# Kernel tuning notes

Hardware: AMD Instinct MI355X
Metric: run time of the kernel (lower is better)

Reference implementation:

```python
import jax, jax.numpy as jnp
import numpy as np

B, T, D, H, L = 32, 1024, 512, 512, 2
OUT = 512 * 2  # output_size is doubled in setup() (bidirectional)


def setup_inputs() -> dict:
    key = jax.random.key(0)
    ks = jax.random.split(key, 9)
    s = 1.0 / np.sqrt(H)
    return {
        "x": jax.random.normal(ks[0], (B, T, D), jnp.float32),
        "h0": jnp.zeros((L, B, H), jnp.float32),
        "c0": jnp.zeros((L, B, H), jnp.float32),
        # stacked LSTM weights, gate order (i, f, g, o) as in flax LSTMCell
        "Wi_f": jax.random.normal(ks[1], (L, D, 4 * H), jnp.float32) * s,
        "Wh_f": jax.random.normal(ks[2], (L, H, 4 * H), jnp.float32) * s,
        "b_f": jnp.zeros((L, 4 * H), jnp.float32),
        "Wi_b": jax.random.normal(ks[3], (L, D, 4 * H), jnp.float32) * s,
        "Wh_b": jax.random.normal(ks[4], (L, H, 4 * H), jnp.float32) * s,
        "b_b": jnp.zeros((L, 4 * H), jnp.float32),
        "W_out": jax.random.normal(ks[5], (2 * H, OUT), jnp.float32) * s,
        "b_out": jnp.zeros((OUT,), jnp.float32),
    }


def _lstm_layer(xs, h0, c0, Wi, Wh, b):
    # xs: [T, B, Din]; scans the sequential recurrence
    def step(carry, x_t):
        h, c = carry
        gates = x_t @ Wi + h @ Wh + b  # [B, 4H]
        i, f, g, o = jnp.split(gates, 4, axis=-1)
        c = jax.nn.sigmoid(f) * c + jax.nn.sigmoid(i) * jnp.tanh(g)
        h = jax.nn.sigmoid(o) * jnp.tanh(c)
        return (h, c), h

    _, hs = jax.lax.scan(step, (h0, c0), xs)
    return hs  # [T, B, H]


def _stack(xs, h0, c0, Wi, Wh, b):
    h = xs
    for l in range(Wi.shape[0]):  # small fixed layer loop
        h = _lstm_layer(h, h0[l], c0[l], Wi[l], Wh[l], b[l])
    return h


def reference(x, h0, c0, Wi_f, Wh_f, b_f, Wi_b, Wh_b, b_b, W_out, b_out):
    xs = jnp.swapaxes(x, 0, 1)  # [T, B, D]
    hf = _stack(xs, h0, c0, Wi_f, Wh_f, b_f)                # forward in time
    hb = _stack(xs[::-1], h0, c0, Wi_b, Wh_b, b_b)[::-1]    # backward in time
    out = jax.nn.relu(jnp.concatenate([hf, hb], axis=-1)) @ W_out + b_out
    return jnp.swapaxes(out, 0, 1)  # [B, T, 2*output_size]
```

## Files before the change

### kernel.cpp

```cpp
#include <hip/hip_runtime.h>
#include <math.h>

typedef __bf16 bf16;
typedef __bf16 bf16x8 __attribute__((ext_vector_type(8)));
typedef float f32x4 __attribute__((ext_vector_type(4)));
typedef int i32x4 __attribute__((ext_vector_type(4)));
typedef unsigned int u32;

#define TT 1024
#define BB 32
#define DD 512
#define HH 512
#define NG4 2048

#define OFF_FLAGS 0ull
#define FLAG_INTS (4u*1024u*64u)
#define OFF_ABORT ((size_t)FLAG_INTS*4ull)
#define OFF_WBT   (OFF_ABORT + 1024ull)
#define OFF_PL    (OFF_WBT + 2097152ull)
#define PL_BYTES  32768ull
#define OFF_H1    (OFF_PL + 4ull*2ull*16ull*PL_BYTES)
#define FULL_ELEM ((size_t)(TT+1)*BB*HH)

#define PLP(gg, pp, slot) (ws + OFF_PL + (((size_t)((gg)*2+(pp))*16 + (size_t)(slot))*PL_BYTES))

__device__ __forceinline__ bf16x8 load16_sc(const void* p) {
  i32x4 r;
  asm volatile("global_load_dwordx4 %0, %1, off sc0 sc1" : "=v"(r) : "v"(p) : "memory");
  return __builtin_bit_cast(bf16x8, r);
}
__device__ __forceinline__ void store_short_sc(void* p, u32 v) {
  asm volatile("global_store_short %0, %1, off sc0 sc1" :: "v"(p), "v"(v) : "memory");
}

__device__ __forceinline__ bool pollrow(int* row, int lane, int* abortf) {
  int it = 0;
  while (true) {
    int v = __hip_atomic_load(row + lane, __ATOMIC_RELAXED, __HIP_MEMORY_SCOPE_AGENT);
    if (__all(v != 0)) return true;
    __builtin_amdgcn_s_sleep(1);
    if ((++it & 1023) == 0) {
      if (it > (1 << 21)) {
        __hip_atomic_store(abortf, 1, __ATOMIC_RELAXED, __HIP_MEMORY_SCOPE_AGENT);
        return false;
      }
      if (__hip_atomic_load(abortf, __ATOMIC_RELAXED, __HIP_MEMORY_SCOPE_AGENT)) return false;
    }
  }
}

__global__ void k_setup(const float* __restrict__ h0,
                        const float* __restrict__ wout,
                        unsigned char* __restrict__ ws) {
  bf16* wbt  = (bf16*)(ws + OFF_WBT);
  int* flags = (int*)(ws + OFF_FLAGS);
  const u32 wcnt = 1024u*1024u;
  const u32 pcnt = 4u*BB*HH;
  const u32 fcnt = FLAG_INTS + 1u;
  const u32 total = wcnt + pcnt + fcnt;
  for (u32 i = blockIdx.x*blockDim.x + threadIdx.x; i < total; i += gridDim.x*blockDim.x) {
    if (i < wcnt) {
      u32 j = i >> 10, k = i & 1023u;
      wbt[(size_t)j*1024u + k] = (bf16)wout[(size_t)k*1024u + j];
    } else if (i < wcnt + pcnt) {
      u32 t = i - wcnt;
      u32 g = t >> 14;
      u32 rem = t & 16383u;
      u32 l = g >> 1;
      float v = h0[(size_t)l*(BB*HH) + rem];
      bf16 hi = (bf16)v;
      bf16 lo = (bf16)(v - (float)hi);
      ((bf16*)PLP(g, 0, 15))[rem] = hi;
      ((bf16*)PLP(g, 1, 15))[rem] = lo;
    } else {
      flags[i - wcnt - pcnt] = 0;
    }
  }
}

__launch_bounds__(256, 1)
__global__ void k_rnn(const float* __restrict__ x,
                      const float* __restrict__ c0,
                      const float* __restrict__ Wi_f, const float* __restrict__ Wh_f, const float* __restrict__ b_f,
                      const float* __restrict__ Wi_b, const float* __restrict__ Wh_b, const float* __restrict__ b_b,
                      unsigned char* __restrict__ ws) {
  __shared__ float gb[4][32][33];
  __shared__ int sab;

  const int bid = blockIdx.x;
  const int g = bid & 3;
  const int w = bid >> 2;
  const int l = g >> 1, d = g & 1;
  const int tid = threadIdx.x;
  const int lane = tid & 63;
  const int q = tid >> 6;

  const float* Wi   = (d ? Wi_b : Wi_f) + (size_t)l*DD*NG4;
  const float* Wh   = (d ? Wh_b : Wh_f) + (size_t)l*HH*NG4;
  const float* bias = (d ? b_b : b_f) + (size_t)l*NG4;

  int* flags  = (int*)(ws + OFF_FLAGS);
  int* abortf = flags + FLAG_INTS;

  const int lrow = lane & 15;
  const int kr0  = (lane >> 4) * 8;

  bf16x8 BWi[4][2], BWh[4][2], BWlo[4][2];
#pragma unroll
  for (int j = 0; j < 4; ++j) {
    int k0 = (q*4 + j)*32 + kr0;
#pragma unroll
    for (int nt = 0; nt < 2; ++nt) {
      int cc = nt*16 + lrow;
      int unit = cc >> 2, gate = cc & 3;
      int Jcol = gate*512 + w*8 + unit;
      bf16x8 ai, ah, al;
#pragma unroll
      for (int e = 0; e < 8; ++e) {
        float wi = Wi[(size_t)(k0+e)*NG4 + Jcol];
        float wh = Wh[(size_t)(k0+e)*NG4 + Jcol];
        ai[e] = (bf16)wi;
        bf16 hh = (bf16)wh;
        ah[e] = hh;
        al[e] = (bf16)(wh - (float)hh);
      }
      BWi[j][nt] = ai; BWh[j][nt] = ah; BWlo[j][nt] = al;
    }
  }

  u32 aoff[4][2];
#pragma unroll
  for (int j = 0; j < 4; ++j)
#pragma unroll
    for (int mt = 0; mt < 2; ++mt)
      aoff[j][mt] = (u32)((((mt*16 + lrow)*512) + (q*4 + j)*32 + kr0) * 2);

  const int bthr = tid >> 3, uthr = tid & 7;
  const int hu = w*8 + uthr;
  float cst = c0[((size_t)l*BB + bthr)*HH + hu];
  const float bgi = bias[hu], bgf = bias[512+hu], bgg = bias[1024+hu], bgo = bias[1536+hu];

  if (tid == 0) sab = 0;
  __syncthreads();

  for (int s = 0; s < TT; ++s) {
    const int slot_w = s & 15;
    const int slot_r = (s + 15) & 15;

    if (l == 1) {
      if (q == 1) { if (!pollrow(flags + ((size_t)d*1024 + s)*64, lane, abortf)) sab = 1; }
      __syncthreads();
    }

    f32x4 acc[2][2];
#pragma unroll
    for (int mt = 0; mt < 2; ++mt)
#pragma unroll
      for (int nt = 0; nt < 2; ++nt) acc[mt][nt] = (f32x4){0.f,0.f,0.f,0.f};

    if (l == 0) {
      const int t_time = d ? (TT-1-s) : s;
      bf16x8 Ax[4][2];
#pragma unroll
      for (int j = 0; j < 4; ++j)
#pragma unroll
        for (int mt = 0; mt < 2; ++mt) {
          const float* px = x + ((size_t)(mt*16 + lrow)*TT + t_time)*DD + (q*4 + j)*32 + kr0;
          float4 a  = *(const float4*)px;
          float4 b4 = *(const float4*)(px + 4);
          bf16x8 v = { (bf16)a.x,(bf16)a.y,(bf16)a.z,(bf16)a.w,
                       (bf16)b4.x,(bf16)b4.y,(bf16)b4.z,(bf16)b4.w };
          Ax[j][mt] = v;
        }
      if (q == 0 && s > 0)   { if (!pollrow(flags + ((size_t)g*1024 + (s-1))*64, lane, abortf)) sab = 1; }
      if (q == 1 && s >= 16) { if (!pollrow(flags + ((size_t)(2+d)*1024 + (s-16))*64, lane, abortf)) sab = 1; }
#pragma unroll
      for (int j = 0; j < 4; ++j)
#pragma unroll
        for (int mt = 0; mt < 2; ++mt)
#pragma unroll
          for (int nt = 0; nt < 2; ++nt)
            acc[mt][nt] = __builtin_amdgcn_mfma_f32_16x16x32_bf16(Ax[j][mt], BWi[j][nt], acc[mt][nt], 0, 0, 0);
    } else {
      const unsigned char* xb = PLP(d, 0, slot_w);
      bf16x8 Ax[4][2];
#pragma unroll
      for (int j = 0; j < 4; ++j)
#pragma unroll
        for (int mt = 0; mt < 2; ++mt)
          Ax[j][mt] = load16_sc(xb + aoff[j][mt]);
      if (q == 0 && s > 0) { if (!pollrow(flags + ((size_t)g*1024 + (s-1))*64, lane, abortf)) sab = 1; }
      asm volatile("s_waitcnt vmcnt(0)" ::: "memory");
      __builtin_amdgcn_sched_barrier(0);
#pragma unroll
      for (int j = 0; j < 4; ++j)
#pragma unroll
        for (int mt = 0; mt < 2; ++mt)
#pragma unroll
          for (int nt = 0; nt < 2; ++nt)
            acc[mt][nt] = __builtin_amdgcn_mfma_f32_16x16x32_bf16(Ax[j][mt], BWi[j][nt], acc[mt][nt], 0, 0, 0);
    }
    __syncthreads();
    if (sab) return;

    const unsigned char* hb = PLP(g, 0, slot_r);
    const unsigned char* lb = PLP(g, 1, slot_r);
    bf16x8 Ahi[4][2], Alo[4][2];
#pragma unroll
    for (int j = 0; j < 4; ++j)
#pragma unroll
      for (int mt = 0; mt < 2; ++mt) {
        Ahi[j][mt] = load16_sc(hb + aoff[j][mt]);
        Alo[j][mt] = load16_sc(lb + aoff[j][mt]);
      }
    asm volatile("s_waitcnt vmcnt(0)" ::: "memory");
    __builtin_amdgcn_sched_barrier(0);
#pragma unroll
    for (int j = 0; j < 4; ++j) {
#pragma unroll
      for (int mt = 0; mt < 2; ++mt)
#pragma unroll
        for (int nt = 0; nt < 2; ++nt)
          acc[mt][nt] = __builtin_amdgcn_mfma_f32_16x16x32_bf16(Ahi[j][mt], BWh[j][nt], acc[mt][nt], 0, 0, 0);
#pragma unroll
      for (int mt = 0; mt < 2; ++mt)
#pragma unroll
        for (int nt = 0; nt < 2; ++nt)
          acc[mt][nt] = __builtin_amdgcn_mfma_f32_16x16x32_bf16(Alo[j][mt], BWh[j][nt], acc[mt][nt], 0, 0, 0);
#pragma unroll
      for (int mt = 0; mt < 2; ++mt)
#pragma unroll
        for (int nt = 0; nt < 2; ++nt)
          acc[mt][nt] = __builtin_amdgcn_mfma_f32_16x16x32_bf16(Ahi[j][mt], BWlo[j][nt], acc[mt][nt], 0, 0, 0);
    }

#pragma unroll
    for (int mt = 0; mt < 2; ++mt)
#pragma unroll
      for (int nt = 0; nt < 2; ++nt)
#pragma unroll
        for (int r = 0; r < 4; ++r)
          gb[q][mt*16 + (lane>>4)*4 + r][nt*16 + lrow] = acc[mt][nt][r];
    __syncthreads();

    float gi = bgi, gf = bgf, gg2 = bgg, go = bgo;
#pragma unroll
    for (int qq = 0; qq < 4; ++qq) {
      gi  += gb[qq][bthr][uthr*4 + 0];
      gf  += gb[qq][bthr][uthr*4 + 1];
      gg2 += gb[qq][bthr][uthr*4 + 2];
      go  += gb[qq][bthr][uthr*4 + 3];
    }
    float si = 1.f/(1.f + __expf(-gi));
    float sf = 1.f/(1.f + __expf(-gf));
    float so = 1.f/(1.f + __expf(-go));
    cst = sf*cst + si*tanhf(gg2);
    float h = so*tanhf(cst);

    bf16 hh = (bf16)h;
    bf16 hl = (bf16)(h - (float)hh);
    u32 off2 = (u32)((bthr*512 + hu) * 2);
    store_short_sc((void*)(PLP(g, 0, slot_w) + off2), (u32)__builtin_bit_cast(unsigned short, hh));
    store_short_sc((void*)(PLP(g, 1, slot_w) + off2), (u32)__builtin_bit_cast(unsigned short, hl));
    if (l == 1) {
      float* H1 = (float*)(ws + OFF_H1) + (size_t)d*FULL_ELEM;
      H1[((size_t)(s+1)*BB + bthr)*HH + hu] = h;
    }
    asm volatile("s_waitcnt vmcnt(0)" ::: "memory");
    __syncthreads();
    if (tid == 0)
      __hip_atomic_store(flags + ((size_t)g*1024 + s)*64 + w, 1,
                         __ATOMIC_RELAXED, __HIP_MEMORY_SCOPE_AGENT);
  }
}

#define SWZG(row, bc) ((u32)(row)*128u + ((u32)(bc) ^ ((((u32)(row))&7u)<<4)))

__launch_bounds__(256, 2)
__global__ void k_out(const unsigned char* __restrict__ ws,
                      const float* __restrict__ bout,
                      float* __restrict__ out) {
  __shared__ unsigned char As[64*128];
  __shared__ unsigned char Bs[128*128];
  const float* Hf = (const float*)(ws + OFF_H1);
  const float* Hb = Hf + FULL_ELEM;
  const bf16* wbt = (const bf16*)(ws + OFF_WBT);

  const int m0 = blockIdx.x * 64;
  const int j0 = blockIdx.y * 128;
  const int tid = threadIdx.x, lane = tid & 63, q = tid >> 6;
  const int b = m0 >> 10;
  const int t0 = m0 & 1023;

  f32x4 acc[2][4];
#pragma unroll
  for (int mi = 0; mi < 2; ++mi)
#pragma unroll
    for (int ni = 0; ni < 4; ++ni) acc[mi][ni] = (f32x4){0.f,0.f,0.f,0.f};

  for (int kb = 0; kb < 16; ++kb) {
#pragma unroll
    for (int it = 0; it < 2; ++it) {
      int row = tid >> 2;
      int chunk = (tid & 3) + it*4;
      int k0 = kb*64 + chunk*8;
      int t = t0 + row;
      const float* src = (k0 < 512)
        ? (Hf + ((size_t)(t+1)*BB + b)*HH + k0)
        : (Hb + ((size_t)(TT-t)*BB + b)*HH + (k0-512));
      float4 fa = *(const float4*)src;
      float4 fb = *(const float4*)(src + 4);
      bf16x8 v = { (bf16)fmaxf(fa.x,0.f),(bf16)fmaxf(fa.y,0.f),(bf16)fmaxf(fa.z,0.f),(bf16)fmaxf(fa.w,0.f),
                   (bf16)fmaxf(fb.x,0.f),(bf16)fmaxf(fb.y,0.f),(bf16)fmaxf(fb.z,0.f),(bf16)fmaxf(fb.w,0.f) };
      *(bf16x8*)(As + SWZG(row, chunk*16)) = v;
    }
#pragma unroll
    for (int it = 0; it < 4; ++it) {
      int j = (tid >> 3) + it*32;
      int chunk = tid & 7;
      int k0 = kb*64 + chunk*8;
      bf16x8 v = *(const bf16x8*)(wbt + (size_t)(j0+j)*1024 + k0);
      *(bf16x8*)(Bs + SWZG(j, chunk*16)) = v;
    }
    __syncthreads();
    const int mrow = (q & 1)*32;
    const int nc0 = (q >> 1)*64;
#pragma unroll
    for (int ks = 0; ks < 2; ++ks) {
      u32 koff = (u32)(ks*32 + (lane>>4)*8) * 2u;
      bf16x8 afr[2];
#pragma unroll
      for (int mi = 0; mi < 2; ++mi)
        afr[mi] = *(const bf16x8*)(As + SWZG(mrow + mi*16 + (lane&15), koff));
#pragma unroll
      for (int ni = 0; ni < 4; ++ni) {
        bf16x8 bfr = *(const bf16x8*)(Bs + SWZG(nc0 + ni*16 + (lane&15), koff));
#pragma unroll
        for (int mi = 0; mi < 2; ++mi)
          acc[mi][ni] = __builtin_amdgcn_mfma_f32_16x16x32_bf16(afr[mi], bfr, acc[mi][ni], 0, 0, 0);
      }
    }
    __syncthreads();
  }
#pragma unroll
  for (int ni = 0; ni < 4; ++ni) {
    int col = j0 + (q >> 1)*64 + ni*16 + (lane & 15);
    float bv = bout[col];
#pragma unroll
    for (int mi = 0; mi < 2; ++mi) {
#pragma unroll
      for (int r = 0; r < 4; ++r) {
        int m = m0 + (q & 1)*32 + mi*16 + (lane >> 4)*4 + r;
        out[(size_t)m*1024 + col] = acc[mi][ni][r] + bv;
      }
    }
  }
}

extern "C" void kernel_launch(void* const* d_in, const int* in_sizes, int n_in,
                              void* d_out, int out_size, void* d_ws, size_t ws_size,
                              hipStream_t stream) {
  const float* x    = (const float*)d_in[0];
  const float* h0   = (const float*)d_in[1];
  const float* c0   = (const float*)d_in[2];
  const float* Wi_f = (const float*)d_in[3];
  const float* Wh_f = (const float*)d_in[4];
  const float* b_f  = (const float*)d_in[5];
  const float* Wi_b = (const float*)d_in[6];
  const float* Wh_b = (const float*)d_in[7];
  const float* b_b  = (const float*)d_in[8];
  const float* Wo   = (const float*)d_in[9];
  const float* bo   = (const float*)d_in[10];
  unsigned char* ws = (unsigned char*)d_ws;
  float* out = (float*)d_out;

  hipLaunchKernelGGL(k_setup, dim3(256), dim3(256), 0, stream, h0, Wo, ws);

  void* args[] = { (void*)&x, (void*)&c0, (void*)&Wi_f, (void*)&Wh_f, (void*)&b_f,
                   (void*)&Wi_b, (void*)&Wh_b, (void*)&b_b, (void*)&ws };
  hipError_t e = hipLaunchCooperativeKernel((const void*)k_rnn, dim3(256), dim3(256),
                                            args, 0, stream);
  if (e != hipSuccess) {
    hipLaunchKernelGGL(k_rnn, dim3(256), dim3(256), 0, stream,
                       x, c0, Wi_f, Wh_f, b_f, Wi_b, Wh_b, b_b, ws);
  }

  hipLaunchKernelGGL(k_out, dim3(512, 8), dim3(256), 0, stream,
                     (const unsigned char*)ws, bo, out);
}
```

Measured before the change: 6.435 ms.

## Replace flag-based step sync with parity-tagged data polling and restructure RNN kernel

```diff
diff --git a/kernel.cpp b/kernel.cpp
--- a/kernel.cpp
+++ b/kernel.cpp
@@ -6,250 +6,365 @@
 typedef float f32x4 __attribute__((ext_vector_type(4)));
 typedef int i32x4 __attribute__((ext_vector_type(4)));
 typedef unsigned int u32;
+typedef unsigned short u16;
 
 #define TT 1024
 #define BB 32
-#define DD 512
 #define HH 512
-#define NG4 2048
-
-#define OFF_FLAGS 0ull
-#define FLAG_INTS (4u*1024u*64u)
-#define OFF_ABORT ((size_t)FLAG_INTS*4ull)
-#define OFF_WBT   (OFF_ABORT + 1024ull)
-#define OFF_PL    (OFF_WBT + 2097152ull)
-#define PL_BYTES  32768ull
-#define OFF_H1    (OFF_PL + 4ull*2ull*16ull*PL_BYTES)
-#define FULL_ELEM ((size_t)(TT+1)*BB*HH)
-
-#define PLP(gg, pp, slot) (ws + OFF_PL + (((size_t)((gg)*2+(pp))*16 + (size_t)(slot))*PL_BYTES))
-
-__device__ __forceinline__ bf16x8 load16_sc(const void* p) {
-  i32x4 r;
-  asm volatile("global_load_dwordx4 %0, %1, off sc0 sc1" : "=v"(r) : "v"(p) : "memory");
-  return __builtin_bit_cast(bf16x8, r);
-}
-__device__ __forceinline__ void store_short_sc(void* p, u32 v) {
-  asm volatile("global_store_short %0, %1, off sc0 sc1" :: "v"(p), "v"(v) : "memory");
-}
-
-__device__ __forceinline__ bool pollrow(int* row, int lane, int* abortf) {
-  int it = 0;
-  while (true) {
-    int v = __hip_atomic_load(row + lane, __ATOMIC_RELAXED, __HIP_MEMORY_SCOPE_AGENT);
-    if (__all(v != 0)) return true;
-    __builtin_amdgcn_s_sleep(1);
-    if ((++it & 1023) == 0) {
-      if (it > (1 << 21)) {
-        __hip_atomic_store(abortf, 1, __ATOMIC_RELAXED, __HIP_MEMORY_SCOPE_AGENT);
-        return false;
-      }
-      if (__hip_atomic_load(abortf, __ATOMIC_RELAXED, __HIP_MEMORY_SCOPE_AGENT)) return false;
+
+#define OFF_CTL   0ull
+#define OFF_WBT   4096ull
+#define OFF_FRAG  (OFF_WBT + 2097152ull)
+#define FRAG_B    8388608ull
+#define OFF_PL    (OFF_FRAG + 3ull*FRAG_B)
+#define PL_SLOT   65536ull
+#define PL_GRP    (16ull*PL_SLOT)
+#define OFF_H1    (OFF_PL + 4ull*PL_GRP)
+#define H1_ELEM   ((size_t)(TT+1)*BB*HH)
+
+__global__ void k_setup(const float* __restrict__ h0, const float* __restrict__ wout,
+                        const float* __restrict__ Wi_f, const float* __restrict__ Wh_f,
+                        const float* __restrict__ Wi_b, const float* __restrict__ Wh_b,
+                        unsigned char* __restrict__ ws) {
+  const u32 N0 = 1048576, N1 = 1048576, N3 = 2097152, N4 = 2097152, N5 = 16;
+  const u32 total = N0 + N1 + N3 + N4 + N5;
+  for (u32 i = blockIdx.x*blockDim.x + threadIdx.x; i < total; i += gridDim.x*blockDim.x) {
+    if (i < N0) {
+      u32 jj = i >> 10, kk = i & 1023u;
+      ((bf16*)(ws + OFF_WBT))[(size_t)jj*1024 + kk] = (bf16)wout[(size_t)kk*1024 + jj];
+    } else if (i < N0 + N1) {
+      u32 t = i - N0;
+      u32 g = t >> 18, rem = t & 262143u;
+      u32 slot = rem >> 14, r = rem & 16383u;
+      u32 word = 0x00010000u;
+      if (slot == 15) {
+        u32 b = r >> 9, u = r & 511u, l = g >> 1;
+        float v = h0[((size_t)l*BB + b)*HH + u];
+        bf16 hi = (bf16)v;
+        bf16 lo = (bf16)(v - (float)hi);
+        u16 lob = (u16)((__builtin_bit_cast(u16, lo) & 0xFFFEu) | 1u);
+        word = (u32)__builtin_bit_cast(u16, hi) | ((u32)lob << 16);
+      }
+      *(u32*)(ws + OFF_PL + (size_t)g*PL_GRP + (size_t)slot*PL_SLOT + (size_t)r*4) = word;
+    } else if (i < N0 + N1 + N3 + N4) {
+      u32 t = i - N0 - N1;
+      int isWh = (t >= N3);
+      if (isWh) t -= N3;
+      u32 e2 = t & 3u, lane = (t>>2)&63u, j = (t>>8)&1u, nt = (t>>9)&3u;
+      u32 q = (t>>11)&7u, w2 = (t>>14)&31u, g = (t>>19)&3u;
+      u32 l = g >> 1, d = g & 1;
+      u32 lrow = lane & 15u;
+      u32 cc = nt*16 + lrow;
+      u32 unit = cc >> 2, gate = cc & 3u;
+      u32 J = gate*512 + w2*16 + unit;
+      u32 k = q*64 + j*32 + (lane>>4)*8 + e2*2;
+      const float* src = isWh ? ((d ? Wh_b : Wh_f) + (size_t)l*HH*2048)
+                              : ((d ? Wi_b : Wi_f) + (size_t)l*HH*2048);
+      float v0 = src[(size_t)k*2048 + J];
+      float v1 = src[(size_t)(k+1)*2048 + J];
+      size_t fo = (((((((size_t)g*32+w2)*8+q)*4+nt)*2+j)*64+lane)*8 + e2*2);
+      if (!isWh) {
+        u32 word = (u32)__builtin_bit_cast(u16,(bf16)v0) | ((u32)__builtin_bit_cast(u16,(bf16)v1) << 16);
+        *(u32*)(ws + OFF_FRAG + fo*2) = word;
+      } else {
+        bf16 h0b = (bf16)v0, h1b = (bf16)v1;
+        bf16 l0b = (bf16)(v0 - (float)h0b), l1b = (bf16)(v1 - (float)h1b);
+        *(u32*)(ws + OFF_FRAG + FRAG_B + fo*2) =
+          (u32)__builtin_bit_cast(u16,h0b) | ((u32)__builtin_bit_cast(u16,h1b) << 16);
+        *(u32*)(ws + OFF_FRAG + 2ull*FRAG_B + fo*2) =
+          (u32)__builtin_bit_cast(u16,l0b) | ((u32)__builtin_bit_cast(u16,l1b) << 16);
+      }
+    } else {
+      u32 t = i - (N0+N1+N3+N4);
+      int* pc = (int*)(ws + OFF_CTL);
+      if (t == 0) pc[0] = 0;
+      else if (t <= 2) pc[t] = -1;
+      else pc[t] = 0;
     }
   }
 }
 
-__global__ void k_setup(const float* __restrict__ h0,
-                        const float* __restrict__ wout,
-                        unsigned char* __restrict__ ws) {
-  bf16* wbt  = (bf16*)(ws + OFF_WBT);
-  int* flags = (int*)(ws + OFF_FLAGS);
-  const u32 wcnt = 1024u*1024u;
-  const u32 pcnt = 4u*BB*HH;
-  const u32 fcnt = FLAG_INTS + 1u;
-  const u32 total = wcnt + pcnt + fcnt;
-  for (u32 i = blockIdx.x*blockDim.x + threadIdx.x; i < total; i += gridDim.x*blockDim.x) {
-    if (i < wcnt) {
-      u32 j = i >> 10, k = i & 1023u;
-      wbt[(size_t)j*1024u + k] = (bf16)wout[(size_t)k*1024u + j];
-    } else if (i < wcnt + pcnt) {
-      u32 t = i - wcnt;
-      u32 g = t >> 14;
-      u32 rem = t & 16383u;
-      u32 l = g >> 1;
-      float v = h0[(size_t)l*(BB*HH) + rem];
-      bf16 hi = (bf16)v;
-      bf16 lo = (bf16)(v - (float)hi);
-      ((bf16*)PLP(g, 0, 15))[rem] = hi;
-      ((bf16*)PLP(g, 1, 15))[rem] = lo;
-    } else {
-      flags[i - wcnt - pcnt] = 0;
-    }
-  }
-}
-
-__launch_bounds__(256, 1)
-__global__ void k_rnn(const float* __restrict__ x,
-                      const float* __restrict__ c0,
-                      const float* __restrict__ Wi_f, const float* __restrict__ Wh_f, const float* __restrict__ b_f,
-                      const float* __restrict__ Wi_b, const float* __restrict__ Wh_b, const float* __restrict__ b_b,
+#define LD16(dst, p) asm volatile("global_load_dwordx4 %0, %1, off sc0 sc1" : "=v"(dst) : "v"(p) : "memory")
+#define ST4(p, v)    asm volatile("global_store_dword %0, %1, off sc0 sc1" :: "v"(p), "v"(v) : "memory")
+#define WAIT0() do { asm volatile("s_waitcnt vmcnt(0)" ::: "memory"); __builtin_amdgcn_sched_barrier(0); } while (0)
+
+__launch_bounds__(512)
+__global__ void k_rnn(const float* __restrict__ x, const float* __restrict__ c0,
+                      const float* __restrict__ b_f, const float* __restrict__ b_b,
                       unsigned char* __restrict__ ws) {
-  __shared__ float gb[4][32][33];
-  __shared__ int sab;
+  __shared__ float gb[4][32][68];
+  __shared__ int sdead;
 
   const int bid = blockIdx.x;
-  const int g = bid & 3;
-  const int w = bid >> 2;
+  if (bid & 1) return;
+  const int g = (bid >> 1) & 3;
+  const int w = bid >> 3;
   const int l = g >> 1, d = g & 1;
   const int tid = threadIdx.x;
   const int lane = tid & 63;
   const int q = tid >> 6;
-
-  const float* Wi   = (d ? Wi_b : Wi_f) + (size_t)l*DD*NG4;
-  const float* Wh   = (d ? Wh_b : Wh_f) + (size_t)l*HH*NG4;
-  const float* bias = (d ? b_b : b_f) + (size_t)l*NG4;
-
-  int* flags  = (int*)(ws + OFF_FLAGS);
-  int* abortf = flags + FLAG_INTS;
-
   const int lrow = lane & 15;
-  const int kr0  = (lane >> 4) * 8;
+  const int ksub = (lane >> 4) * 8;
+
+  int* ctl    = (int*)(ws + OFF_CTL);
+  int* abortf = ctl;
+  int* prog1  = ctl + 1;
+
+  if (tid == 0) sdead = 0;
 
   bf16x8 BWi[4][2], BWh[4][2], BWlo[4][2];
 #pragma unroll
-  for (int j = 0; j < 4; ++j) {
-    int k0 = (q*4 + j)*32 + kr0;
-#pragma unroll
-    for (int nt = 0; nt < 2; ++nt) {
-      int cc = nt*16 + lrow;
-      int unit = cc >> 2, gate = cc & 3;
-      int Jcol = gate*512 + w*8 + unit;
-      bf16x8 ai, ah, al;
-#pragma unroll
-      for (int e = 0; e < 8; ++e) {
-        float wi = Wi[(size_t)(k0+e)*NG4 + Jcol];
-        float wh = Wh[(size_t)(k0+e)*NG4 + Jcol];
-        ai[e] = (bf16)wi;
-        bf16 hh = (bf16)wh;
-        ah[e] = hh;
-        al[e] = (bf16)(wh - (float)hh);
-      }
-      BWi[j][nt] = ai; BWh[j][nt] = ah; BWlo[j][nt] = al;
+  for (int nt = 0; nt < 4; ++nt)
+#pragma unroll
+    for (int j = 0; j < 2; ++j) {
+      size_t fo = (((((((size_t)g*32+w)*8+q)*4+nt)*2+j)*64+lane)*8) * 2;
+      BWi[nt][j]  = *(const bf16x8*)(ws + OFF_FRAG + fo);
+      BWh[nt][j]  = *(const bf16x8*)(ws + OFF_FRAG + FRAG_B + fo);
+      BWlo[nt][j] = *(const bf16x8*)(ws + OFF_FRAG + 2ull*FRAG_B + fo);
+    }
+
+  const int bthr = tid >> 4, uthr = tid & 15;
+  const int hu = w*16 + uthr;
+  float cst = c0[((size_t)l*BB + bthr)*HH + hu];
+  const float* bias = (d ? b_b : b_f) + (size_t)l*2048;
+  const float bgi = bias[hu], bgf = bias[512+hu], bgg = bias[1024+hu], bgo = bias[1536+hu];
+
+  unsigned char* plMain = ws + OFF_PL + (size_t)g*PL_GRP;
+  unsigned char* plIn   = ws + OFF_PL + (size_t)d*PL_GRP;
+  bf16* H1p = (bf16*)(ws + OFF_H1) + (size_t)d*H1_ELEM;
+
+  u32 ao[2][2];
+#pragma unroll
+  for (int j = 0; j < 2; ++j)
+#pragma unroll
+    for (int mt = 0; mt < 2; ++mt)
+      ao[j][mt] = (u32)((((mt*16 + lrow)*512) + q*64 + j*32 + ksub) * 4);
+
+  __syncthreads();
+
+  float4 xr[8];
+  i32x4  xm[4][2];
+  if (l == 0) {
+    int t0i = d ? (TT-1) : 0;
+#pragma unroll
+    for (int p = 0; p < 4; ++p) {
+      int j = p >> 1, mt = p & 1;
+      const float* px = x + (((size_t)(mt*16+lrow))*TT + t0i)*512 + q*64 + j*32 + ksub;
+      xr[p*2]   = *(const float4*)px;
+      xr[p*2+1] = *(const float4*)(px + 4);
+    }
+  } else {
+#pragma unroll
+    for (int p = 0; p < 4; ++p) {
+      int j = p >> 1, mt = p & 1;
+      const unsigned char* pp = plIn + ao[j][mt];
+      LD16(xm[p][0], pp);
+      LD16(xm[p][1], pp + 16);
     }
   }
 
-  u32 aoff[4][2];
-#pragma unroll
-  for (int j = 0; j < 4; ++j)
-#pragma unroll
-    for (int mt = 0; mt < 2; ++mt)
-      aoff[j][mt] = (u32)((((mt*16 + lrow)*512) + (q*4 + j)*32 + kr0) * 2);
-
-  const int bthr = tid >> 3, uthr = tid & 7;
-  const int hu = w*8 + uthr;
-  float cst = c0[((size_t)l*BB + bthr)*HH + hu];
-  const float bgi = bias[hu], bgf = bias[512+hu], bgg = bias[1024+hu], bgo = bias[1536+hu];
-
-  if (tid == 0) sab = 0;
-  __syncthreads();
+  int prog_cache = -1000000;
+  int dead = 0;
 
   for (int s = 0; s < TT; ++s) {
     const int slot_w = s & 15;
-    const int slot_r = (s + 15) & 15;
-
-    if (l == 1) {
-      if (q == 1) { if (!pollrow(flags + ((size_t)d*1024 + s)*64, lane, abortf)) sab = 1; }
-      __syncthreads();
-    }
-
-    f32x4 acc[2][2];
+    const u32 par_w = (u32)((s >> 4) & 1);
+    const u32 par_r = (u32)(((s - 1) >> 4) & 1);
+    const unsigned char* slotR = plMain + (size_t)((s - 1) & 15)*PL_SLOT;
+
+    i32x4 hw[4][2];
+    {
+      const u32 expw = par_r << 16;
+      int pit = 0;
+      while (true) {
+#pragma unroll
+        for (int p = 0; p < 4; ++p) {
+          int j = p >> 1, mt = p & 1;
+          LD16(hw[p][0], slotR + ao[j][mt]);
+          LD16(hw[p][1], slotR + ao[j][mt] + 16);
+        }
+        WAIT0();
+        if (dead) break;
+        u32 m = 0;
+#pragma unroll
+        for (int p = 0; p < 4; ++p)
+#pragma unroll
+          for (int hh = 0; hh < 2; ++hh)
+#pragma unroll
+            for (int e = 0; e < 4; ++e)
+              m |= ((u32)hw[p][hh][e]) ^ expw;
+        if (__all((int)(((m >> 16) & 1u) == 0u))) break;
+        ++pit;
+        if (pit > 64) __builtin_amdgcn_s_sleep(1);
+        if ((pit & 255) == 0) {
+          if (sdead || __hip_atomic_load(abortf, __ATOMIC_RELAXED, __HIP_MEMORY_SCOPE_AGENT)) dead = 1;
+          if (pit > (1 << 20)) {
+            __hip_atomic_store(abortf, 1, __ATOMIC_RELAXED, __HIP_MEMORY_SCOPE_AGENT);
+            sdead = 1; dead = 1;
+          }
+        }
+      }
+    }
+
+    f32x4 acc[2][4];
 #pragma unroll
     for (int mt = 0; mt < 2; ++mt)
 #pragma unroll
-      for (int nt = 0; nt < 2; ++nt) acc[mt][nt] = (f32x4){0.f,0.f,0.f,0.f};
+      for (int nt = 0; nt < 4; ++nt) acc[mt][nt] = (f32x4){0.f, 0.f, 0.f, 0.f};
 
     if (l == 0) {
-      const int t_time = d ? (TT-1-s) : s;
-      bf16x8 Ax[4][2];
-#pragma unroll
-      for (int j = 0; j < 4; ++j)
-#pragma unroll
-        for (int mt = 0; mt < 2; ++mt) {
-          const float* px = x + ((size_t)(mt*16 + lrow)*TT + t_time)*DD + (q*4 + j)*32 + kr0;
-          float4 a  = *(const float4*)px;
-          float4 b4 = *(const float4*)(px + 4);
-          bf16x8 v = { (bf16)a.x,(bf16)a.y,(bf16)a.z,(bf16)a.w,
-                       (bf16)b4.x,(bf16)b4.y,(bf16)b4.z,(bf16)b4.w };
-          Ax[j][mt] = v;
+#pragma unroll
+      for (int p = 0; p < 4; ++p) {
+        int j = p >> 1, mt = p & 1;
+        float4 a = xr[p*2], b4 = xr[p*2+1];
+        bf16x8 ax = { (bf16)a.x,(bf16)a.y,(bf16)a.z,(bf16)a.w,
+                      (bf16)b4.x,(bf16)b4.y,(bf16)b4.z,(bf16)b4.w };
+#pragma unroll
+        for (int nt = 0; nt < 4; ++nt)
+          acc[mt][nt] = __builtin_amdgcn_mfma_f32_16x16x32_bf16(ax, BWi[nt][j], acc[mt][nt], 0, 0, 0);
+      }
+      if (s + 1 < TT) {
+        int tn = d ? (TT-2-s) : (s+1);
+#pragma unroll
+        for (int p = 0; p < 4; ++p) {
+          int j = p >> 1, mt = p & 1;
+          const float* px = x + (((size_t)(mt*16+lrow))*TT + tn)*512 + q*64 + j*32 + ksub;
+          xr[p*2]   = *(const float4*)px;
+          xr[p*2+1] = *(const float4*)(px + 4);
         }
-      if (q == 0 && s > 0)   { if (!pollrow(flags + ((size_t)g*1024 + (s-1))*64, lane, abortf)) sab = 1; }
-      if (q == 1 && s >= 16) { if (!pollrow(flags + ((size_t)(2+d)*1024 + (s-16))*64, lane, abortf)) sab = 1; }
-#pragma unroll
-      for (int j = 0; j < 4; ++j)
-#pragma unroll
-        for (int mt = 0; mt < 2; ++mt)
-#pragma unroll
-          for (int nt = 0; nt < 2; ++nt)
-            acc[mt][nt] = __builtin_amdgcn_mfma_f32_16x16x32_bf16(Ax[j][mt], BWi[j][nt], acc[mt][nt], 0, 0, 0);
+      }
     } else {
-      const unsigned char* xb = PLP(d, 0, slot_w);
-      bf16x8 Ax[4][2];
-#pragma unroll
-      for (int j = 0; j < 4; ++j)
-#pragma unroll
-        for (int mt = 0; mt < 2; ++mt)
-          Ax[j][mt] = load16_sc(xb + aoff[j][mt]);
-      if (q == 0 && s > 0) { if (!pollrow(flags + ((size_t)g*1024 + (s-1))*64, lane, abortf)) sab = 1; }
-      asm volatile("s_waitcnt vmcnt(0)" ::: "memory");
-      __builtin_amdgcn_sched_barrier(0);
-#pragma unroll
-      for (int j = 0; j < 4; ++j)
-#pragma unroll
-        for (int mt = 0; mt < 2; ++mt)
-#pragma unroll
-          for (int nt = 0; nt < 2; ++nt)
-            acc[mt][nt] = __builtin_amdgcn_mfma_f32_16x16x32_bf16(Ax[j][mt], BWi[j][nt], acc[mt][nt], 0, 0, 0);
-    }
+      const u32 expx = ((u32)((s >> 4) & 1)) << 16;
+      u32 mx = 0;
+#pragma unroll
+      for (int p = 0; p < 4; ++p)
+#pragma unroll
+        for (int hh = 0; hh < 2; ++hh)
+#pragma unroll
+          for (int e = 0; e < 4; ++e)
+            mx |= ((u32)xm[p][hh][e]) ^ expx;
+      if (!__all((int)(((mx >> 16) & 1u) == 0u)) && !dead) {
+        const unsigned char* xs = plIn + (size_t)slot_w*PL_SLOT;
+        int pit = 0;
+        while (true) {
+#pragma unroll
+          for (int p = 0; p < 4; ++p) {
+            int j = p >> 1, mt = p & 1;
+            LD16(xm[p][0], xs + ao[j][mt]);
+            LD16(xm[p][1], xs + ao[j][mt] + 16);
+          }
+          WAIT0();
+          mx = 0;
+#pragma unroll
+          for (int p = 0; p < 4; ++p)
+#pragma unroll
+            for (int hh = 0; hh < 2; ++hh)
+#pragma unroll
+              for (int e = 0; e < 4; ++e)
+                mx |= ((u32)xm[p][hh][e]) ^ expx;
+          if (__all((int)(((mx >> 16) & 1u) == 0u))) break;
+          ++pit;
+          if (pit > 16) __builtin_amdgcn_s_sleep(1);
+          if ((pit & 255) == 0) {
+            if (sdead || __hip_atomic_load(abortf, __ATOMIC_RELAXED, __HIP_MEMORY_SCOPE_AGENT)) { dead = 1; break; }
+            if (pit > (1 << 20)) {
+              __hip_atomic_store(abortf, 1, __ATOMIC_RELAXED, __HIP_MEMORY_SCOPE_AGENT);
+              sdead = 1; dead = 1; break;
+            }
+          }
+        }
+      }
+#pragma unroll
+      for (int p = 0; p < 4; ++p) {
+        int j = p >> 1, mt = p & 1;
+        i32x4 w0 = xm[p][0], w1 = xm[p][1];
+        i32x4 hi4;
+        hi4[0] = (int)(((u32)w0[0] & 0xFFFFu) | ((u32)w0[1] << 16));
+        hi4[1] = (int)(((u32)w0[2] & 0xFFFFu) | ((u32)w0[3] << 16));
+        hi4[2] = (int)(((u32)w1[0] & 0xFFFFu) | ((u32)w1[1] << 16));
+        hi4[3] = (int)(((u32)w1[2] & 0xFFFFu) | ((u32)w1[3] << 16));
+        bf16x8 ax = __builtin_bit_cast(bf16x8, hi4);
+#pragma unroll
+        for (int nt = 0; nt < 4; ++nt)
+          acc[mt][nt] = __builtin_amdgcn_mfma_f32_16x16x32_bf16(ax, BWi[nt][j], acc[mt][nt], 0, 0, 0);
+      }
+      if (s + 1 < TT) {
+        const unsigned char* xs2 = plIn + (size_t)((s + 1) & 15)*PL_SLOT;
+#pragma unroll
+        for (int p = 0; p < 4; ++p) {
+          int j = p >> 1, mt = p & 1;
+          LD16(xm[p][0], xs2 + ao[j][mt]);
+          LD16(xm[p][1], xs2 + ao[j][mt] + 16);
+        }
+      }
+    }
+
+#pragma unroll
+    for (int p = 0; p < 4; ++p) {
+      int j = p >> 1, mt = p & 1;
+      i32x4 w0 = hw[p][0], w1 = hw[p][1];
+      i32x4 hi4, lo4;
+      hi4[0] = (int)(((u32)w0[0] & 0xFFFFu) | ((u32)w0[1] << 16));
+      hi4[1] = (int)(((u32)w0[2] & 0xFFFFu) | ((u32)w0[3] << 16));
+      hi4[2] = (int)(((u32)w1[0] & 0xFFFFu) | ((u32)w1[1] << 16));
+      hi4[3] = (int)(((u32)w1[2] & 0xFFFFu) | ((u32)w1[3] << 16));
+      lo4[0] = (int)(((u32)w0[0] >> 16) | ((u32)w0[1] & 0xFFFF0000u));
+      lo4[1] = (int)(((u32)w0[2] >> 16) | ((u32)w0[3] & 0xFFFF0000u));
+      lo4[2] = (int)(((u32)w1[0] >> 16) | ((u32)w1[1] & 0xFFFF0000u));
+      lo4[3] = (int)(((u32)w1[2] >> 16) | ((u32)w1[3] & 0xFFFF0000u));
+      bf16x8 ahi = __builtin_bit_cast(bf16x8, hi4);
+      bf16x8 alo = __builtin_bit_cast(bf16x8, lo4);
+#pragma unroll
+      for (int nt = 0; nt < 4; ++nt) {
+        acc[mt][nt] = __builtin_amdgcn_mfma_f32_16x16x32_bf16(ahi, BWh[nt][j],  acc[mt][nt], 0, 0, 0);
+        acc[mt][nt] = __builtin_amdgcn_mfma_f32_16x16x32_bf16(alo, BWh[nt][j],  acc[mt][nt], 0, 0, 0);
+        acc[mt][nt] = __builtin_amdgcn_mfma_f32_16x16x32_bf16(ahi, BWlo[nt][j], acc[mt][nt], 0, 0, 0);
+      }
+    }
+
+    if (l == 0 && q == 0 && s >= 16) {
+      int pit = 0;
+      while (prog_cache < s - 15 && !dead) {
+        prog_cache = __hip_atomic_load(prog1 + d, __ATOMIC_RELAXED, __HIP_MEMORY_SCOPE_AGENT);
+        if (prog_cache < s - 15) {
+          __builtin_amdgcn_s_sleep(2);
+          if ((++pit & 255) == 0) {
+            if (sdead || __hip_atomic_load(abortf, __ATOMIC_RELAXED, __HIP_MEMORY_SCOPE_AGENT)) dead = 1;
+            if (pit > (1 << 20)) { __hip_atomic_store(abortf, 1, __ATOMIC_RELAXED, __HIP_MEMORY_SCOPE_AGENT); sdead = 1; dead = 1; }
+          }
+        }
+      }
+    }
+
     __syncthreads();
-    if (sab) return;
-
-    const unsigned char* hb = PLP(g, 0, slot_r);
-    const unsigned char* lb = PLP(g, 1, slot_r);
-    bf16x8 Ahi[4][2], Alo[4][2];
-#pragma unroll
-    for (int j = 0; j < 4; ++j)
-#pragma unroll
-      for (int mt = 0; mt < 2; ++mt) {
-        Ahi[j][mt] = load16_sc(hb + aoff[j][mt]);
-        Alo[j][mt] = load16_sc(lb + aoff[j][mt]);
-      }
-    asm volatile("s_waitcnt vmcnt(0)" ::: "memory");
-    __builtin_amdgcn_sched_barrier(0);
-#pragma unroll
-    for (int j = 0; j < 4; ++j) {
+    if (q >= 4) {
 #pragma unroll
       for (int mt = 0; mt < 2; ++mt)
 #pragma unroll
-        for (int nt = 0; nt < 2; ++nt)
-          acc[mt][nt] = __builtin_amdgcn_mfma_f32_16x16x32_bf16(Ahi[j][mt], BWh[j][nt], acc[mt][nt], 0, 0, 0);
+        for (int nt = 0; nt < 4; ++nt)
+#pragma unroll
+          for (int r = 0; r < 4; ++r)
+            gb[q-4][mt*16 + (lane>>4)*4 + r][nt*16 + lrow] = acc[mt][nt][r];
+    }
+    __syncthreads();
+    if (q < 4) {
 #pragma unroll
       for (int mt = 0; mt < 2; ++mt)
 #pragma unroll
-        for (int nt = 0; nt < 2; ++nt)
-          acc[mt][nt] = __builtin_amdgcn_mfma_f32_16x16x32_bf16(Alo[j][mt], BWh[j][nt], acc[mt][nt], 0, 0, 0);
-#pragma unroll
-      for (int mt = 0; mt < 2; ++mt)
-#pragma unroll
-        for (int nt = 0; nt < 2; ++nt)
-          acc[mt][nt] = __builtin_amdgcn_mfma_f32_16x16x32_bf16(Ahi[j][mt], BWlo[j][nt], acc[mt][nt], 0, 0, 0);
-    }
-
-#pragma unroll
-    for (int mt = 0; mt < 2; ++mt)
-#pragma unroll
-      for (int nt = 0; nt < 2; ++nt)
-#pragma unroll
-        for (int r = 0; r < 4; ++r)
-          gb[q][mt*16 + (lane>>4)*4 + r][nt*16 + lrow] = acc[mt][nt][r];
+        for (int nt = 0; nt < 4; ++nt)
+#pragma unroll
+          for (int r = 0; r < 4; ++r) {
+            float* c = &gb[q][mt*16 + (lane>>4)*4 + r][nt*16 + lrow];
+            *c = *c + acc[mt][nt][r];
+          }
+    }
     __syncthreads();
 
     float gi = bgi, gf = bgf, gg2 = bgg, go = bgo;
 #pragma unroll
     for (int qq = 0; qq < 4; ++qq) {
-      gi  += gb[qq][bthr][uthr*4 + 0];
-      gf  += gb[qq][bthr][uthr*4 + 1];
-      gg2 += gb[qq][bthr][uthr*4 + 2];
-      go  += gb[qq][bthr][uthr*4 + 3];
+      f32x4 pv = *(const f32x4*)&gb[qq][bthr][uthr*4];
+      gi += pv[0]; gf += pv[1]; gg2 += pv[2]; go += pv[3];
     }
     float si = 1.f/(1.f + __expf(-gi));
     float sf = 1.f/(1.f + __expf(-gf));
@@ -257,20 +372,17 @@
     cst = sf*cst + si*tanhf(gg2);
     float h = so*tanhf(cst);
 
-    bf16 hh = (bf16)h;
-    bf16 hl = (bf16)(h - (float)hh);
-    u32 off2 = (u32)((bthr*512 + hu) * 2);
-    store_short_sc((void*)(PLP(g, 0, slot_w) + off2), (u32)__builtin_bit_cast(unsigned short, hh));
-    store_short_sc((void*)(PLP(g, 1, slot_w) + off2), (u32)__builtin_bit_cast(unsigned short, hl));
+    bf16 hhv = (bf16)h;
+    bf16 hlv = (bf16)(h - (float)hhv);
+    u16 lob = (u16)((__builtin_bit_cast(u16, hlv) & 0xFFFEu) | (u16)par_w);
+    u32 word = (u32)__builtin_bit_cast(u16, hhv) | ((u32)lob << 16);
+    unsigned char* wp = plMain + (size_t)slot_w*PL_SLOT + (size_t)(bthr*512 + hu)*4;
+    ST4(wp, word);
     if (l == 1) {
-      float* H1 = (float*)(ws + OFF_H1) + (size_t)d*FULL_ELEM;
-      H1[((size_t)(s+1)*BB + bthr)*HH + hu] = h;
-    }
-    asm volatile("s_waitcnt vmcnt(0)" ::: "memory");
-    __syncthreads();
-    if (tid == 0)
-      __hip_atomic_store(flags + ((size_t)g*1024 + s)*64 + w, 1,
-                         __ATOMIC_RELAXED, __HIP_MEMORY_SCOPE_AGENT);
+      H1p[((size_t)(s+1)*BB + bthr)*HH + hu] = hhv;
+      if (w == 0 && tid == 0)
+        __hip_atomic_store(prog1 + d, s, __ATOMIC_RELAXED, __HIP_MEMORY_SCOPE_AGENT);
+    }
   }
 }
 
@@ -282,8 +394,8 @@
                       float* __restrict__ out) {
   __shared__ unsigned char As[64*128];
   __shared__ unsigned char Bs[128*128];
-  const float* Hf = (const float*)(ws + OFF_H1);
-  const float* Hb = Hf + FULL_ELEM;
+  const bf16* Hf = (const bf16*)(ws + OFF_H1);
+  const bf16* Hb = Hf + H1_ELEM;
   const bf16* wbt = (const bf16*)(ws + OFF_WBT);
 
   const int m0 = blockIdx.x * 64;
@@ -305,13 +417,12 @@
       int chunk = (tid & 3) + it*4;
       int k0 = kb*64 + chunk*8;
       int t = t0 + row;
-      const float* src = (k0 < 512)
+      const bf16* src = (k0 < 512)
         ? (Hf + ((size_t)(t+1)*BB + b)*HH + k0)
-        : (Hb + ((size_t)(TT-t)*BB + b)*HH + (k0-512));
-      float4 fa = *(const float4*)src;
-      float4 fb = *(const float4*)(src + 4);
-      bf16x8 v = { (bf16)fmaxf(fa.x,0.f),(bf16)fmaxf(fa.y,0.f),(bf16)fmaxf(fa.z,0.f),(bf16)fmaxf(fa.w,0.f),
-                   (bf16)fmaxf(fb.x,0.f),(bf16)fmaxf(fb.y,0.f),(bf16)fmaxf(fb.z,0.f),(bf16)fmaxf(fb.w,0.f) };
+        : (Hb + ((size_t)(TT - t)*BB + b)*HH + (k0 - 512));
+      bf16x8 v = *(const bf16x8*)src;
+#pragma unroll
+      for (int e = 0; e < 8; ++e) { if ((float)v[e] < 0.f) v[e] = (bf16)0.f; }
       *(bf16x8*)(As + SWZG(row, chunk*16)) = v;
     }
 #pragma unroll
@@ -374,15 +485,14 @@
   unsigned char* ws = (unsigned char*)d_ws;
   float* out = (float*)d_out;
 
-  hipLaunchKernelGGL(k_setup, dim3(256), dim3(256), 0, stream, h0, Wo, ws);
-
-  void* args[] = { (void*)&x, (void*)&c0, (void*)&Wi_f, (void*)&Wh_f, (void*)&b_f,
-                   (void*)&Wi_b, (void*)&Wh_b, (void*)&b_b, (void*)&ws };
-  hipError_t e = hipLaunchCooperativeKernel((const void*)k_rnn, dim3(256), dim3(256),
+  hipLaunchKernelGGL(k_setup, dim3(2048), dim3(256), 0, stream,
+                     h0, Wo, Wi_f, Wh_f, Wi_b, Wh_b, ws);
+
+  void* args[] = { (void*)&x, (void*)&c0, (void*)&b_f, (void*)&b_b, (void*)&ws };
+  hipError_t e = hipLaunchCooperativeKernel((const void*)k_rnn, dim3(256), dim3(512),
                                             args, 0, stream);
   if (e != hipSuccess) {
-    hipLaunchKernelGGL(k_rnn, dim3(256), dim3(256), 0, stream,
-                       x, c0, Wi_f, Wh_f, b_f, Wi_b, Wh_b, b_b, ws);
+    hipLaunchKernelGGL(k_rnn, dim3(256), dim3(512), 0, stream, x, c0, b_f, b_b, ws);
   }
 
   hipLaunchKernelGGL(k_out, dim3(512, 8), dim3(256), 0, stream,
```

Result: slower. 17.80 ms (+176.7%).
